# Kernel tuning notes

Measured on AMD Instinct MI355X. Metric: run time of the kernel, lower is better.

The kernel has to match this reference:

```python
import jax, jax.numpy as jnp
import numpy as np

N_NODES = 100000
N_EDGES = 1600000
IN_C, HID_C, OUT_C = 64, 128, 64


def _sage_conv(x, src, dst, Wl, bl, Wr, n_nodes):
    # PyG SAGEConv (mean aggr): out = lin_l(mean_{j in N(i)} x_j) + lin_r(x_i)
    msg = x[src]  # [E, C] gather
    agg = jax.ops.segment_sum(msg, dst, num_segments=n_nodes)
    deg = jax.ops.segment_sum(jnp.ones((src.shape[0],), x.dtype), dst, num_segments=n_nodes)
    agg = agg / jnp.maximum(deg, 1.0)[:, None]
    return agg @ Wl + bl + x @ Wr


def setup_inputs() -> dict:
    key = jax.random.key(0)
    ks = jax.random.split(key, 16)
    x = jax.random.normal(ks[0], (N_NODES, IN_C), dtype=jnp.float32)
    edge_index = jax.random.randint(ks[1], (2, N_EDGES), 0, N_NODES, dtype=jnp.int64)
    s = 0.05
    return {
        "x": x,
        "edge_index": edge_index,
        # conv1: SAGEConv(IN_C, HID_C)
        "Wl1": jax.random.normal(ks[2], (IN_C, HID_C), jnp.float32) * s,
        "bl1": jnp.zeros((HID_C,), jnp.float32),
        "Wr1": jax.random.normal(ks[3], (IN_C, HID_C), jnp.float32) * s,
        # conv2: SAGEConv(HID_C, OUT_C)
        "Wl2": jax.random.normal(ks[4], (HID_C, OUT_C), jnp.float32) * s,
        "bl2": jnp.zeros((OUT_C,), jnp.float32),
        "Wr2": jax.random.normal(ks[5], (HID_C, OUT_C), jnp.float32) * s,
        # classifier MLP: OUT_C -> HID_C -> HID_C//2 -> 1
        "Wc1": jax.random.normal(ks[6], (OUT_C, HID_C), jnp.float32) * s,
        "bc1": jnp.zeros((HID_C,), jnp.float32),
        "Wc2": jax.random.normal(ks[7], (HID_C, HID_C // 2), jnp.float32) * s,
        "bc2": jnp.zeros((HID_C // 2,), jnp.float32),
        "Wc3": jax.random.normal(ks[8], (HID_C // 2, 1), jnp.float32) * s,
        "bc3": jnp.zeros((1,), jnp.float32),
    }


def reference(x, edge_index, Wl1, bl1, Wr1, Wl2, bl2, Wr2, Wc1, bc1, Wc2, bc2, Wc3, bc3):
    src, dst = edge_index[0], edge_index[1]
    n = x.shape[0]
    h = _sage_conv(x, src, dst, Wl1, bl1, Wr1, n)
    h = jax.nn.relu(h)  # dropout is identity in eval mode
    embeddings = _sage_conv(h, src, dst, Wl2, bl2, Wr2, n)
    # classifier head
    c = jax.nn.relu(embeddings @ Wc1 + bc1)
    c = jax.nn.relu(c @ Wc2 + bc2)
    fraud_probs = jax.nn.sigmoid(c @ Wc3 + bc3)
    return embeddings, fraud_probs
```

## Files before the change

kernel.cpp:

```cpp
#include <hip/hip_runtime.h>
#include <math.h>

#define N_NODES 100000
#define N_EDGES 1600000
#define NBKT    391
#define BCAP    5120
#define EPB     4096
#define NBLKA   391

using short8  = __attribute__((ext_vector_type(8))) short;
using float4v = __attribute__((ext_vector_type(4))) float;

__device__ inline unsigned short f2bf(float f) {
    unsigned int u = __float_as_uint(f);
    u += 0x7fffu + ((u >> 16) & 1u);
    return (unsigned short)(u >> 16);
}
__device__ inline float bflo(unsigned int v) { return __uint_as_float(v << 16); }
__device__ inline float bfhi(unsigned int v) { return __uint_as_float(v & 0xffff0000u); }

__global__ void prep_weights(const float* __restrict__ Wl1, const float* __restrict__ Wr1,
                             const float* __restrict__ Wl2, const float* __restrict__ Wr2,
                             const float* __restrict__ Wc1, const float* __restrict__ Wc2,
                             unsigned short* __restrict__ w1, unsigned short* __restrict__ w2,
                             unsigned short* __restrict__ wcls1, unsigned short* __restrict__ wcls2) {
    int i = blockIdx.x * 256 + threadIdx.x;
    if (i < 16384) {
        int n = i >> 7, k = i & 127;
        float v = (k < 64) ? Wl1[k * 128 + n] : Wr1[(k - 64) * 128 + n];
        w1[i] = f2bf(v);
    } else if (i < 32768) {
        int j = i - 16384; int n = j >> 7, k = j & 127;
        float v = (n < 64) ? Wl2[k * 64 + n] : Wr2[k * 64 + (n - 64)];
        w2[j] = f2bf(v);
    } else if (i < 40960) {
        int j = i - 32768; int n = j >> 6, k = j & 63;
        wcls1[j] = f2bf(Wc1[k * 128 + n]);
    } else {
        int j = i - 40960; int n = j >> 7, k = j & 127;
        wcls2[j] = f2bf(Wc2[k * 64 + n]);
    }
}

__global__ void f32_to_bf16x4(const float* __restrict__ src, unsigned short* __restrict__ dst) {
    int i = blockIdx.x * 256 + threadIdx.x;
    float4 v = *(const float4*)(src + (long)i * 4);
    uint2 o;
    o.x = (unsigned)f2bf(v.x) | ((unsigned)f2bf(v.y) << 16);
    o.y = (unsigned)f2bf(v.z) | ((unsigned)f2bf(v.w) << 16);
    *(uint2*)(dst + (long)i * 4) = o;
}

__global__ __launch_bounds__(256) void binA(const int* __restrict__ esrc,
                                            const int* __restrict__ edst,
                                            int* __restrict__ bcnt,
                                            unsigned* __restrict__ stage) {
    __shared__ int hist[NBKT];
    __shared__ int rbase[NBKT];
    int t = threadIdx.x;
    for (int i = t; i < NBKT; i += 256) hist[i] = 0;
    __syncthreads();
    int e0 = blockIdx.x * EPB;
    int e1 = e0 + EPB; if (e1 > N_EDGES) e1 = N_EDGES;
    unsigned pk[16];
    int bn[16];
#pragma unroll
    for (int j = 0; j < 16; j++) {
        int e = e0 + j * 256 + t;
        bn[j] = -1;
        if (e < N_EDGES && e < e1) {
            int d = edst[e];
            int s = esrc[e];
            int b = d >> 8;
            pk[j] = (unsigned)s | ((unsigned)(d & 255) << 24);
            bn[j] = b;
            atomicAdd(&hist[b], 1);
        }
    }
    __syncthreads();
    for (int i = t; i < NBKT; i += 256) {
        int c = hist[i];
        rbase[i] = c ? atomicAdd(&bcnt[i], c) : 0;
        hist[i] = 0;
    }
    __syncthreads();
#pragma unroll
    for (int j = 0; j < 16; j++) {
        if (bn[j] >= 0) {
            int b = bn[j];
            int slot = rbase[b] + atomicAdd(&hist[b], 1);
            if (slot < BCAP)
                stage[(long)b * BCAP + slot] = pk[j];
        }
    }
}

__global__ void binScan(const int* __restrict__ bcnt, int* __restrict__ bbase,
                        int* __restrict__ off) {
    __shared__ int s[512];
    int t = threadIdx.x;
    int v = (t < NBKT) ? bcnt[t] : 0;
    s[t] = v;
    __syncthreads();
    for (int st = 1; st < 512; st <<= 1) {
        int a = (t >= st) ? s[t - st] : 0;
        __syncthreads();
        s[t] += a;
        __syncthreads();
    }
    if (t < NBKT) bbase[t] = s[t] - v;
    if (t == 0) off[N_NODES] = N_EDGES;
}

__global__ __launch_bounds__(256) void binB(const int* __restrict__ bcnt,
                                            const int* __restrict__ bbase,
                                            const unsigned* __restrict__ stage,
                                            int* __restrict__ off, int* __restrict__ bucket) {
    __shared__ int hist[256];
    __shared__ int scn[256];
    __shared__ int lbase[256];
    int b = blockIdx.x, t = threadIdx.x;
    int cnt = bcnt[b];
    if (cnt > BCAP) cnt = BCAP;
    int base = bbase[b];
    hist[t] = 0;
    __syncthreads();
    const unsigned* sp = stage + (long)b * BCAP;
    unsigned pk[20];
    int nv = 0;
#pragma unroll
    for (int j = 0; j < 20; j++) {
        int i = j * 256 + t;
        if (i < cnt) {
            pk[j] = sp[i];
            atomicAdd(&hist[pk[j] >> 24], 1);
            nv = j + 1;
        }
    }
    __syncthreads();
    int v = hist[t];
    scn[t] = v;
    __syncthreads();
    for (int st = 1; st < 256; st <<= 1) {
        int a = (t >= st) ? scn[t - st] : 0;
        __syncthreads();
        scn[t] += a;
        __syncthreads();
    }
    lbase[t] = scn[t] - v;
    int node = b * 256 + t;
    if (node < N_NODES) off[node] = base + lbase[t];
    hist[t] = 0;
    __syncthreads();
#pragma unroll
    for (int j = 0; j < 20; j++) {
        if (j < nv) {
            unsigned p = pk[j];
            int ln = p >> 24;
            int slot = atomicAdd(&hist[ln], 1);
            bucket[base + lbase[ln] + slot] = (int)(p & 0xFFFFFFu);
        }
    }
}

__global__ __launch_bounds__(256, 8) void gather_b(
        const unsigned short* __restrict__ y, const int* __restrict__ off,
        const int* __restrict__ bucket, unsigned short* __restrict__ outb) {
    int node = __builtin_amdgcn_readfirstlane(blockIdx.x * 4 + (threadIdx.x >> 6));
    int lane = threadIdx.x & 63;
    int g = lane >> 3, c8 = lane & 7;
    int e0 = off[node], e1 = off[node + 1];
    float a[8] = {0.f, 0.f, 0.f, 0.f, 0.f, 0.f, 0.f, 0.f};
    for (int base = e0; base < e1; base += 32) {
        uint4 v[4];
#pragma unroll
        for (int h = 0; h < 4; h++) {
            int idx = base + h * 8 + g;
            if (idx < e1) {
                int s = bucket[idx];
                v[h] = *(const uint4*)(y + (long)s * 64 + c8 * 8);
            } else {
                v[h] = (uint4){0u, 0u, 0u, 0u};
            }
        }
#pragma unroll
        for (int h = 0; h < 4; h++) {
            a[0] += bflo(v[h].x); a[1] += bfhi(v[h].x);
            a[2] += bflo(v[h].y); a[3] += bfhi(v[h].y);
            a[4] += bflo(v[h].z); a[5] += bfhi(v[h].z);
            a[6] += bflo(v[h].w); a[7] += bfhi(v[h].w);
        }
    }
#pragma unroll
    for (int j = 0; j < 8; j++) {
        a[j] += __shfl_xor(a[j], 8);
        a[j] += __shfl_xor(a[j], 16);
        a[j] += __shfl_xor(a[j], 32);
    }
    if (g == 0) {
        float sc = 1.f / fmaxf((float)(e1 - e0), 1.f);
        uint4 o;
        o.x = (unsigned)f2bf(a[0]*sc) | ((unsigned)f2bf(a[1]*sc) << 16);
        o.y = (unsigned)f2bf(a[2]*sc) | ((unsigned)f2bf(a[3]*sc) << 16);
        o.z = (unsigned)f2bf(a[4]*sc) | ((unsigned)f2bf(a[5]*sc) << 16);
        o.w = (unsigned)f2bf(a[6]*sc) | ((unsigned)f2bf(a[7]*sc) << 16);
        *(uint4*)(outb + (long)node * 64 + c8 * 8) = o;
    }
}

__global__ __launch_bounds__(256, 8) void gather_badd(
        const unsigned short* __restrict__ y, const int* __restrict__ off,
        const int* __restrict__ bucket, const float* __restrict__ add,
        float* __restrict__ out) {
    int node = __builtin_amdgcn_readfirstlane(blockIdx.x * 4 + (threadIdx.x >> 6));
    int lane = threadIdx.x & 63;
    int g = lane >> 3, c8 = lane & 7;
    int e0 = off[node], e1 = off[node + 1];
    float a[8] = {0.f, 0.f, 0.f, 0.f, 0.f, 0.f, 0.f, 0.f};
    for (int base = e0; base < e1; base += 32) {
        uint4 v[4];
#pragma unroll
        for (int h = 0; h < 4; h++) {
            int idx = base + h * 8 + g;
            if (idx < e1) {
                int s = bucket[idx];
                v[h] = *(const uint4*)(y + (long)s * 64 + c8 * 8);
            } else {
                v[h] = (uint4){0u, 0u, 0u, 0u};
            }
        }
#pragma unroll
        for (int h = 0; h < 4; h++) {
            a[0] += bflo(v[h].x); a[1] += bfhi(v[h].x);
            a[2] += bflo(v[h].y); a[3] += bfhi(v[h].y);
            a[4] += bflo(v[h].z); a[5] += bfhi(v[h].z);
            a[6] += bflo(v[h].w); a[7] += bfhi(v[h].w);
        }
    }
#pragma unroll
    for (int j = 0; j < 8; j++) {
        a[j] += __shfl_xor(a[j], 8);
        a[j] += __shfl_xor(a[j], 16);
        a[j] += __shfl_xor(a[j], 32);
    }
    if (g == 0) {
        float sc = 1.f / fmaxf((float)(e1 - e0), 1.f);
        const float4* up = (const float4*)(add + (long)node * 64 + c8 * 8);
        float4 u0 = up[0], u1 = up[1];
        float4 r0 = { a[0]*sc + u0.x, a[1]*sc + u0.y, a[2]*sc + u0.z, a[3]*sc + u0.w };
        float4 r1 = { a[4]*sc + u1.x, a[5]*sc + u1.y, a[6]*sc + u1.z, a[7]*sc + u1.w };
        float4* op = (float4*)(out + (long)node * 64 + c8 * 8);
        op[0] = r0; op[1] = r1;
    }
}

__global__ __launch_bounds__(256, 4) void fused_conv(
        const unsigned short* __restrict__ xb, const unsigned short* __restrict__ aggb,
        const unsigned short* __restrict__ w1, const float* __restrict__ bl1,
        const unsigned short* __restrict__ w2, const float* __restrict__ bl2,
        unsigned short* __restrict__ t2b, float* __restrict__ u) {
    __shared__ __align__(16) unsigned short smemA[64 * 136];
    __shared__ __align__(16) unsigned short smemH[64 * 136];
    unsigned short* sA = smemA;
    unsigned short* sH = smemH;
    float* su = (float*)smemA;
    unsigned short* st2 = smemH;

    int t = threadIdx.x;
    int lane = t & 63;
    int wv = t >> 6;
    int q = lane >> 4, ln = lane & 15;

    long base = (long)blockIdx.x * 4096;
    long maxe = (long)N_NODES * 64 - 8;
#pragma unroll
    for (int it = 0; it < 2; it++) {
        int i = it * 256 + t;
        int m = i >> 3, k8 = (i & 7) * 8;
        long g = base + (long)m * 64 + k8;
        if (g > maxe) g = maxe;
        *(uint4*)(sA + m * 136 + k8)      = *(const uint4*)(aggb + g);
        *(uint4*)(sA + m * 136 + 64 + k8) = *(const uint4*)(xb + g);
    }
    __syncthreads();

    int n0 = wv * 32;
    float4v acc[2][4];
    {
        float b0 = bl1[n0 + ln], b1 = bl1[n0 + 16 + ln];
#pragma unroll
        for (int mi = 0; mi < 4; mi++) {
            acc[0][mi] = (float4v){b0, b0, b0, b0};
            acc[1][mi] = (float4v){b1, b1, b1, b1};
        }
    }
#pragma unroll
    for (int ks = 0; ks < 4; ks++) {
        int k0 = ks * 32 + q * 8;
        short8 bf0 = *(const short8*)(w1 + (long)(n0 + ln) * 128 + k0);
        short8 bf1 = *(const short8*)(w1 + (long)(n0 + 16 + ln) * 128 + k0);
#pragma unroll
        for (int mi = 0; mi < 4; mi++) {
            short8 af = *(const short8*)(sA + (mi * 16 + ln) * 136 + k0);
            acc[0][mi] = __builtin_amdgcn_mfma_f32_16x16x32_bf16(af, bf0, acc[0][mi], 0, 0, 0);
            acc[1][mi] = __builtin_amdgcn_mfma_f32_16x16x32_bf16(af, bf1, acc[1][mi], 0, 0, 0);
        }
    }
#pragma unroll
    for (int j = 0; j < 2; j++)
#pragma unroll
        for (int mi = 0; mi < 4; mi++) {
            int n = n0 + j * 16 + ln;
#pragma unroll
            for (int r = 0; r < 4; r++) {
                int m = mi * 16 + q * 4 + r;
                sH[m * 136 + n] = f2bf(fmaxf(acc[j][mi][r], 0.f));
            }
        }
    __syncthreads();

    float4v acc2[2][4];
    {
        float c0 = (n0 >= 64) ? bl2[n0 - 64 + ln] : 0.f;
        float c1 = (n0 >= 64) ? bl2[n0 - 48 + ln] : 0.f;
#pragma unroll
        for (int mi = 0; mi < 4; mi++) {
            acc2[0][mi] = (float4v){c0, c0, c0, c0};
            acc2[1][mi] = (float4v){c1, c1, c1, c1};
        }
    }
#pragma unroll
    for (int ks = 0; ks < 4; ks++) {
        int k0 = ks * 32 + q * 8;
        short8 bf0 = *(const short8*)(w2 + (long)(n0 + ln) * 128 + k0);
        short8 bf1 = *(const short8*)(w2 + (long)(n0 + 16 + ln) * 128 + k0);
#pragma unroll
        for (int mi = 0; mi < 4; mi++) {
            short8 af = *(const short8*)(sH + (mi * 16 + ln) * 136 + k0);
            acc2[0][mi] = __builtin_amdgcn_mfma_f32_16x16x32_bf16(af, bf0, acc2[0][mi], 0, 0, 0);
            acc2[1][mi] = __builtin_amdgcn_mfma_f32_16x16x32_bf16(af, bf1, acc2[1][mi], 0, 0, 0);
        }
    }
    __syncthreads();

#pragma unroll
    for (int j = 0; j < 2; j++)
#pragma unroll
        for (int mi = 0; mi < 4; mi++) {
            int n = n0 + j * 16 + ln;
#pragma unroll
            for (int r = 0; r < 4; r++) {
                int m = mi * 16 + q * 4 + r;
                if (wv < 2) st2[m * 72 + n] = f2bf(acc2[j][mi][r]);
                else        su[m * 68 + (n - 64)] = acc2[j][mi][r];
            }
        }
    __syncthreads();

    long lim = (long)N_NODES * 64;
    unsigned int* t2u = (unsigned int*)(t2b + base);
#pragma unroll
    for (int it = 0; it < 8; it++) {
        int i = it * 256 + t;
        long g = base + (long)i * 2;
        if (g + 1 < lim) {
            int m = (i * 2) >> 6, n = (i * 2) & 63;
            t2u[i] = (unsigned)st2[m * 72 + n] | ((unsigned)st2[m * 72 + n + 1] << 16);
        }
    }
#pragma unroll
    for (int it = 0; it < 16; it++) {
        int i = it * 256 + t;
        long g = base + i;
        if (g < lim) u[g] = su[(i >> 6) * 68 + (i & 63)];
    }
}

__global__ __launch_bounds__(256, 4) void fused_cls(
        const float* __restrict__ emb,
        const unsigned short* __restrict__ wcls1, const float* __restrict__ bc1,
        const unsigned short* __restrict__ wcls2, const float* __restrict__ bc2,
        const float* __restrict__ wc3, const float* __restrict__ bc3,
        float* __restrict__ probs) {
    __shared__ __align__(16) unsigned short smem[64 * 136];
    __shared__ float psum[4][64];
    unsigned short* sE = smem;
    unsigned short* sC = smem;

    int t = threadIdx.x;
    int wv = t >> 6;
    int lane = t & 63;
    int q = lane >> 4, ln = lane & 15;

    long base = (long)blockIdx.x * 4096;
    long maxe = (long)N_NODES * 64 - 4;
#pragma unroll
    for (int it = 0; it < 4; it++) {
        int i = it * 256 + t;
        int m = i >> 4, k4 = (i & 15) * 4;
        long g = base + (long)m * 64 + k4;
        if (g > maxe) g = maxe;
        float4 v = *(const float4*)(emb + g);
        uint2 o;
        o.x = (unsigned)f2bf(v.x) | ((unsigned)f2bf(v.y) << 16);
        o.y = (unsigned)f2bf(v.z) | ((unsigned)f2bf(v.w) << 16);
        *(uint2*)(sE + m * 72 + k4) = o;
    }
    __syncthreads();

    int n0 = wv * 32;
    float4v acc[2][4];
    {
        float b0 = bc1[n0 + ln], b1 = bc1[n0 + 16 + ln];
#pragma unroll
        for (int mi = 0; mi < 4; mi++) {
            acc[0][mi] = (float4v){b0, b0, b0, b0};
            acc[1][mi] = (float4v){b1, b1, b1, b1};
        }
    }
#pragma unroll
    for (int ks = 0; ks < 2; ks++) {
        int k0 = ks * 32 + q * 8;
        short8 bf0 = *(const short8*)(wcls1 + (long)(n0 + ln) * 64 + k0);
        short8 bf1 = *(const short8*)(wcls1 + (long)(n0 + 16 + ln) * 64 + k0);
#pragma unroll
        for (int mi = 0; mi < 4; mi++) {
            short8 af = *(const short8*)(sE + (mi * 16 + ln) * 72 + k0);
            acc[0][mi] = __builtin_amdgcn_mfma_f32_16x16x32_bf16(af, bf0, acc[0][mi], 0, 0, 0);
            acc[1][mi] = __builtin_amdgcn_mfma_f32_16x16x32_bf16(af, bf1, acc[1][mi], 0, 0, 0);
        }
    }
    __syncthreads();
#pragma unroll
    for (int j = 0; j < 2; j++)
#pragma unroll
        for (int mi = 0; mi < 4; mi++) {
            int n = n0 + j * 16 + ln;
#pragma unroll
            for (int r = 0; r < 4; r++) {
                int m = mi * 16 + q * 4 + r;
                sC[m * 136 + n] = f2bf(fmaxf(acc[j][mi][r], 0.f));
            }
        }
    __syncthreads();

    int n0c = wv * 16;
    float4v acc3[4];
    {
        float b = bc2[n0c + ln];
#pragma unroll
        for (int mi = 0; mi < 4; mi++) acc3[mi] = (float4v){b, b, b, b};
    }
#pragma unroll
    for (int ks = 0; ks < 4; ks++) {
        int k0 = ks * 32 + q * 8;
        short8 bf0 = *(const short8*)(wcls2 + (long)(n0c + ln) * 128 + k0);
#pragma unroll
        for (int mi = 0; mi < 4; mi++) {
            short8 af = *(const short8*)(sC + (mi * 16 + ln) * 136 + k0);
            acc3[mi] = __builtin_amdgcn_mfma_f32_16x16x32_bf16(af, bf0, acc3[mi], 0, 0, 0);
        }
    }
    float w3 = wc3[n0c + ln];
#pragma unroll
    for (int mi = 0; mi < 4; mi++)
#pragma unroll
        for (int r = 0; r < 4; r++) {
            float v = fmaxf(acc3[mi][r], 0.f) * w3;
            v += __shfl_xor(v, 1);
            v += __shfl_xor(v, 2);
            v += __shfl_xor(v, 4);
            v += __shfl_xor(v, 8);
            if (ln == 0) psum[wv][mi * 16 + q * 4 + r] = v;
        }
    __syncthreads();
    if (t < 64) {
        int node = blockIdx.x * 64 + t;
        if (node < N_NODES) {
            float tot = psum[0][t] + psum[1][t] + psum[2][t] + psum[3][t] + bc3[0];
            probs[node] = 1.f / (1.f + expf(-tot));
        }
    }
}

extern "C" void kernel_launch(void* const* d_in, const int* in_sizes, int n_in,
                              void* d_out, int out_size, void* d_ws, size_t ws_size,
                              hipStream_t stream) {
    const float* x   = (const float*)d_in[0];
    const int*   ei  = (const int*)d_in[1];
    const float* Wl1 = (const float*)d_in[2];
    const float* bl1 = (const float*)d_in[3];
    const float* Wr1 = (const float*)d_in[4];
    const float* Wl2 = (const float*)d_in[5];
    const float* bl2 = (const float*)d_in[6];
    const float* Wr2 = (const float*)d_in[7];
    const float* Wc1 = (const float*)d_in[8];
    const float* bc1 = (const float*)d_in[9];
    const float* Wc2 = (const float*)d_in[10];
    const float* bc2 = (const float*)d_in[11];
    const float* Wc3 = (const float*)d_in[12];
    const float* bc3 = (const float*)d_in[13];

    float* out = (float*)d_out;

    int* iw     = (int*)d_ws;
    int* bcnt   = iw;
    int* bbase  = iw + 392;
    int* off    = iw + 1024;
    int* bucket = iw + 1024 + 100352;
    unsigned* stage = (unsigned*)(iw + 1024 + 100352 + N_EDGES);
    size_t ioff = (size_t)(1024 + 100352 + N_EDGES + (long)NBKT * BCAP) * 4;

    char* wsb = (char*)d_ws;
    unsigned short* xb    = (unsigned short*)(wsb + ioff);
    unsigned short* agg1b = xb + 6400000L;
    unsigned short* t2b   = agg1b + 6400000L;
    float*          u     = (float*)(wsb + ioff + 3L * 12800000L);
    unsigned short* w1    = (unsigned short*)(wsb + ioff + 3L * 12800000L + 25600000L);
    unsigned short* w2    = w1 + 16384;
    unsigned short* wcls1 = w2 + 16384;
    unsigned short* wcls2 = wcls1 + 8192;

    float* emb   = out;
    float* probs = out + 6400000L;

    const int* esrc = ei;
    const int* edst = ei + N_EDGES;

    hipMemsetAsync(bcnt, 0, 1024 * sizeof(int), stream);

    prep_weights<<<192, 256, 0, stream>>>(Wl1, Wr1, Wl2, Wr2, Wc1, Wc2,
                                          w1, w2, wcls1, wcls2);
    f32_to_bf16x4<<<6250, 256, 0, stream>>>(x, xb);

    binA<<<NBLKA, 256, 0, stream>>>(esrc, edst, bcnt, stage);
    binScan<<<1, 512, 0, stream>>>(bcnt, bbase, off);
    binB<<<NBKT, 256, 0, stream>>>(bcnt, bbase, stage, off, bucket);

    gather_b<<<25000, 256, 0, stream>>>(xb, off, bucket, agg1b);
    fused_conv<<<1563, 256, 0, stream>>>(xb, agg1b, w1, bl1, w2, bl2, t2b, u);
    gather_badd<<<25000, 256, 0, stream>>>(t2b, off, bucket, u, emb);
    fused_cls<<<1563, 256, 0, stream>>>(emb, wcls1, bc1, wcls2, bc2, Wc3, bc3, probs);
}
```

Before: 269.6 us.

## Pad per-node edge lists to multiples of eight with a zero sentinel row

The CSR build now pads each node's neighbour list to a multiple of eight, filling the gaps with a sentinel index that points at a zeroed row appended to the bf16 feature buffers, and stores the degree separately. The gather kernels can then test bounds per 8-edge group instead of per lane and use 32-bit byte offsets for the row loads. The weight-prep and x-conversion kernels are merged into one launch, which also zeroes the sentinel rows. This adds padding loads of zero rows and a larger bucket buffer in exchange for simpler, branch-uniform gather loops.

```diff
diff --git a/kernel.cpp b/kernel.cpp
--- a/kernel.cpp
+++ b/kernel.cpp
@@ -2,11 +2,14 @@
 #include <math.h>
 
 #define N_NODES 100000
+#define ZERO_NODE 100000
 #define N_EDGES 1600000
 #define NBKT    391
 #define BCAP    5120
 #define EPB     4096
 #define NBLKA   391
+#define PADBKT  1792
+#define BUCKET_CAP (N_EDGES + NBKT * PADBKT)
 
 using short8  = __attribute__((ext_vector_type(8))) short;
 using float4v = __attribute__((ext_vector_type(4))) float;
@@ -19,36 +22,43 @@
 __device__ inline float bflo(unsigned int v) { return __uint_as_float(v << 16); }
 __device__ inline float bfhi(unsigned int v) { return __uint_as_float(v & 0xffff0000u); }
 
-__global__ void prep_weights(const float* __restrict__ Wl1, const float* __restrict__ Wr1,
-                             const float* __restrict__ Wl2, const float* __restrict__ Wr2,
-                             const float* __restrict__ Wc1, const float* __restrict__ Wc2,
-                             unsigned short* __restrict__ w1, unsigned short* __restrict__ w2,
-                             unsigned short* __restrict__ wcls1, unsigned short* __restrict__ wcls2) {
-    int i = blockIdx.x * 256 + threadIdx.x;
-    if (i < 16384) {
-        int n = i >> 7, k = i & 127;
-        float v = (k < 64) ? Wl1[k * 128 + n] : Wr1[(k - 64) * 128 + n];
-        w1[i] = f2bf(v);
-    } else if (i < 32768) {
-        int j = i - 16384; int n = j >> 7, k = j & 127;
-        float v = (n < 64) ? Wl2[k * 64 + n] : Wr2[k * 64 + (n - 64)];
-        w2[j] = f2bf(v);
-    } else if (i < 40960) {
-        int j = i - 32768; int n = j >> 6, k = j & 63;
-        wcls1[j] = f2bf(Wc1[k * 128 + n]);
+__global__ void prep_all(const float* __restrict__ x, unsigned short* __restrict__ xb,
+                         const float* __restrict__ Wl1, const float* __restrict__ Wr1,
+                         const float* __restrict__ Wl2, const float* __restrict__ Wr2,
+                         const float* __restrict__ Wc1, const float* __restrict__ Wc2,
+                         unsigned short* __restrict__ w1, unsigned short* __restrict__ w2,
+                         unsigned short* __restrict__ wcls1, unsigned short* __restrict__ wcls2,
+                         unsigned short* __restrict__ t2b) {
+    int bid = blockIdx.x;
+    int t = threadIdx.x;
+    if (bid < 6250) {
+        int i = bid * 256 + t;
+        float4 v = *(const float4*)(x + (long)i * 4);
+        uint2 o;
+        o.x = (unsigned)f2bf(v.x) | ((unsigned)f2bf(v.y) << 16);
+        o.y = (unsigned)f2bf(v.z) | ((unsigned)f2bf(v.w) << 16);
+        *(uint2*)(xb + (long)i * 4) = o;
+    } else if (bid < 6442) {
+        int i = (bid - 6250) * 256 + t;
+        if (i < 16384) {
+            int n = i >> 7, k = i & 127;
+            float v = (k < 64) ? Wl1[k * 128 + n] : Wr1[(k - 64) * 128 + n];
+            w1[i] = f2bf(v);
+        } else if (i < 32768) {
+            int j = i - 16384; int n = j >> 7, k = j & 127;
+            float v = (n < 64) ? Wl2[k * 64 + n] : Wr2[k * 64 + (n - 64)];
+            w2[j] = f2bf(v);
+        } else if (i < 40960) {
+            int j = i - 32768; int n = j >> 6, k = j & 63;
+            wcls1[j] = f2bf(Wc1[k * 128 + n]);
+        } else {
+            int j = i - 40960; int n = j >> 7, k = j & 127;
+            wcls2[j] = f2bf(Wc2[k * 64 + n]);
+        }
     } else {
-        int j = i - 40960; int n = j >> 7, k = j & 127;
-        wcls2[j] = f2bf(Wc2[k * 64 + n]);
-    }
-}
-
-__global__ void f32_to_bf16x4(const float* __restrict__ src, unsigned short* __restrict__ dst) {
-    int i = blockIdx.x * 256 + threadIdx.x;
-    float4 v = *(const float4*)(src + (long)i * 4);
-    uint2 o;
-    o.x = (unsigned)f2bf(v.x) | ((unsigned)f2bf(v.y) << 16);
-    o.y = (unsigned)f2bf(v.z) | ((unsigned)f2bf(v.w) << 16);
-    *(uint2*)(dst + (long)i * 4) = o;
+        if (t < 32)       ((unsigned*)(xb  + (long)ZERO_NODE * 64))[t]      = 0u;
+        else if (t < 64)  ((unsigned*)(t2b + (long)ZERO_NODE * 64))[t - 32] = 0u;
+    }
 }
 
 __global__ __launch_bounds__(256) void binA(const int* __restrict__ esrc,
@@ -95,8 +105,7 @@
     }
 }
 
-__global__ void binScan(const int* __restrict__ bcnt, int* __restrict__ bbase,
-                        int* __restrict__ off) {
+__global__ void binScan(const int* __restrict__ bcnt, int* __restrict__ pbase) {
     __shared__ int s[512];
     int t = threadIdx.x;
     int v = (t < NBKT) ? bcnt[t] : 0;
@@ -108,21 +117,21 @@
         s[t] += a;
         __syncthreads();
     }
-    if (t < NBKT) bbase[t] = s[t] - v;
-    if (t == 0) off[N_NODES] = N_EDGES;
+    if (t < NBKT) pbase[t] = (s[t] - v) + t * PADBKT;
 }
 
 __global__ __launch_bounds__(256) void binB(const int* __restrict__ bcnt,
-                                            const int* __restrict__ bbase,
+                                            const int* __restrict__ pbase,
                                             const unsigned* __restrict__ stage,
-                                            int* __restrict__ off, int* __restrict__ bucket) {
+                                            int* __restrict__ offp, int* __restrict__ deg,
+                                            int* __restrict__ bucket) {
     __shared__ int hist[256];
     __shared__ int scn[256];
     __shared__ int lbase[256];
     int b = blockIdx.x, t = threadIdx.x;
     int cnt = bcnt[b];
     if (cnt > BCAP) cnt = BCAP;
-    int base = bbase[b];
+    int base = pbase[b];
     hist[t] = 0;
     __syncthreads();
     const unsigned* sp = stage + (long)b * BCAP;
@@ -139,7 +148,8 @@
     }
     __syncthreads();
     int v = hist[t];
-    scn[t] = v;
+    int p8 = (v + 7) & ~7;
+    scn[t] = p8;
     __syncthreads();
     for (int st = 1; st < 256; st <<= 1) {
         int a = (t >= st) ? scn[t - st] : 0;
@@ -147,9 +157,12 @@
         scn[t] += a;
         __syncthreads();
     }
-    lbase[t] = scn[t] - v;
+    lbase[t] = scn[t] - p8;
     int node = b * 256 + t;
-    if (node < N_NODES) off[node] = base + lbase[t];
+    if (node < N_NODES) {
+        offp[node] = base + lbase[t];
+        deg[node]  = v;
+    }
     hist[t] = 0;
     __syncthreads();
 #pragma unroll
@@ -161,24 +174,31 @@
             bucket[base + lbase[ln] + slot] = (int)(p & 0xFFFFFFu);
         }
     }
+    int ps = base + lbase[t] + v;
+    int pe = base + lbase[t] + p8;
+    for (int j = ps; j < pe; j++) bucket[j] = ZERO_NODE;
 }
 
 __global__ __launch_bounds__(256, 8) void gather_b(
-        const unsigned short* __restrict__ y, const int* __restrict__ off,
-        const int* __restrict__ bucket, unsigned short* __restrict__ outb) {
+        const unsigned short* __restrict__ y, const int* __restrict__ offp,
+        const int* __restrict__ deg, const int* __restrict__ bucket,
+        unsigned short* __restrict__ outb) {
     int node = __builtin_amdgcn_readfirstlane(blockIdx.x * 4 + (threadIdx.x >> 6));
     int lane = threadIdx.x & 63;
     int g = lane >> 3, c8 = lane & 7;
-    int e0 = off[node], e1 = off[node + 1];
+    int e0 = offp[node];
+    int dg = deg[node];
+    int e1p = e0 + ((dg + 7) & ~7);
+    const char* yb = (const char*)y;
     float a[8] = {0.f, 0.f, 0.f, 0.f, 0.f, 0.f, 0.f, 0.f};
-    for (int base = e0; base < e1; base += 32) {
+    for (int base = e0; base < e1p; base += 32) {
         uint4 v[4];
 #pragma unroll
         for (int h = 0; h < 4; h++) {
-            int idx = base + h * 8 + g;
-            if (idx < e1) {
-                int s = bucket[idx];
-                v[h] = *(const uint4*)(y + (long)s * 64 + c8 * 8);
+            if (base + h * 8 < e1p) {
+                int s = bucket[base + h * 8 + g];
+                unsigned off32 = ((unsigned)s << 7) + ((unsigned)c8 << 4);
+                v[h] = *(const uint4*)(yb + off32);
             } else {
                 v[h] = (uint4){0u, 0u, 0u, 0u};
             }
@@ -198,7 +218,7 @@
         a[j] += __shfl_xor(a[j], 32);
     }
     if (g == 0) {
-        float sc = 1.f / fmaxf((float)(e1 - e0), 1.f);
+        float sc = 1.f / fmaxf((float)dg, 1.f);
         uint4 o;
         o.x = (unsigned)f2bf(a[0]*sc) | ((unsigned)f2bf(a[1]*sc) << 16);
         o.y = (unsigned)f2bf(a[2]*sc) | ((unsigned)f2bf(a[3]*sc) << 16);
@@ -209,22 +229,25 @@
 }
 
 __global__ __launch_bounds__(256, 8) void gather_badd(
-        const unsigned short* __restrict__ y, const int* __restrict__ off,
-        const int* __restrict__ bucket, const float* __restrict__ add,
-        float* __restrict__ out) {
+        const unsigned short* __restrict__ y, const int* __restrict__ offp,
+        const int* __restrict__ deg, const int* __restrict__ bucket,
+        const float* __restrict__ add, float* __restrict__ out) {
     int node = __builtin_amdgcn_readfirstlane(blockIdx.x * 4 + (threadIdx.x >> 6));
     int lane = threadIdx.x & 63;
     int g = lane >> 3, c8 = lane & 7;
-    int e0 = off[node], e1 = off[node + 1];
+    int e0 = offp[node];
+    int dg = deg[node];
+    int e1p = e0 + ((dg + 7) & ~7);
+    const char* yb = (const char*)y;
     float a[8] = {0.f, 0.f, 0.f, 0.f, 0.f, 0.f, 0.f, 0.f};
-    for (int base = e0; base < e1; base += 32) {
+    for (int base = e0; base < e1p; base += 32) {
         uint4 v[4];
 #pragma unroll
         for (int h = 0; h < 4; h++) {
-            int idx = base + h * 8 + g;
-            if (idx < e1) {
-                int s = bucket[idx];
-                v[h] = *(const uint4*)(y + (long)s * 64 + c8 * 8);
+            if (base + h * 8 < e1p) {
+                int s = bucket[base + h * 8 + g];
+                unsigned off32 = ((unsigned)s << 7) + ((unsigned)c8 << 4);
+                v[h] = *(const uint4*)(yb + off32);
             } else {
                 v[h] = (uint4){0u, 0u, 0u, 0u};
             }
@@ -244,7 +267,7 @@
         a[j] += __shfl_xor(a[j], 32);
     }
     if (g == 0) {
-        float sc = 1.f / fmaxf((float)(e1 - e0), 1.f);
+        float sc = 1.f / fmaxf((float)dg, 1.f);
         const float4* up = (const float4*)(add + (long)node * 64 + c8 * 8);
         float4 u0 = up[0], u1 = up[1];
         float4 r0 = { a[0]*sc + u0.x, a[1]*sc + u0.y, a[2]*sc + u0.z, a[3]*sc + u0.w };
@@ -505,18 +528,20 @@
 
     int* iw     = (int*)d_ws;
     int* bcnt   = iw;
-    int* bbase  = iw + 392;
-    int* off    = iw + 1024;
-    int* bucket = iw + 1024 + 100352;
-    unsigned* stage = (unsigned*)(iw + 1024 + 100352 + N_EDGES);
-    size_t ioff = (size_t)(1024 + 100352 + N_EDGES + (long)NBKT * BCAP) * 4;
+    int* pbase  = iw + 512;
+    int* offp   = iw + 1024;
+    int* deg    = iw + 1024 + 100352;
+    int* bucket = iw + 1024 + 2 * 100352;
+    unsigned* stage = (unsigned*)(bucket + BUCKET_CAP);
+    size_t ioff = ((size_t)(1024 + 2 * 100352 + BUCKET_CAP) + (size_t)NBKT * BCAP) * 4;
+    ioff = (ioff + 127) & ~(size_t)127;
 
     char* wsb = (char*)d_ws;
     unsigned short* xb    = (unsigned short*)(wsb + ioff);
-    unsigned short* agg1b = xb + 6400000L;
+    unsigned short* agg1b = xb + 6400064L;
     unsigned short* t2b   = agg1b + 6400000L;
-    float*          u     = (float*)(wsb + ioff + 3L * 12800000L);
-    unsigned short* w1    = (unsigned short*)(wsb + ioff + 3L * 12800000L + 25600000L);
+    float*          u     = (float*)(t2b + 6400064L);
+    unsigned short* w1    = (unsigned short*)(u + 6400000L);
     unsigned short* w2    = w1 + 16384;
     unsigned short* wcls1 = w2 + 16384;
     unsigned short* wcls2 = wcls1 + 8192;
@@ -529,16 +554,15 @@
 
     hipMemsetAsync(bcnt, 0, 1024 * sizeof(int), stream);
 
-    prep_weights<<<192, 256, 0, stream>>>(Wl1, Wr1, Wl2, Wr2, Wc1, Wc2,
-                                          w1, w2, wcls1, wcls2);
-    f32_to_bf16x4<<<6250, 256, 0, stream>>>(x, xb);
+    prep_all<<<6443, 256, 0, stream>>>(x, xb, Wl1, Wr1, Wl2, Wr2, Wc1, Wc2,
+                                       w1, w2, wcls1, wcls2, t2b);
 
     binA<<<NBLKA, 256, 0, stream>>>(esrc, edst, bcnt, stage);
-    binScan<<<1, 512, 0, stream>>>(bcnt, bbase, off);
-    binB<<<NBKT, 256, 0, stream>>>(bcnt, bbase, stage, off, bucket);
-
-    gather_b<<<25000, 256, 0, stream>>>(xb, off, bucket, agg1b);
+    binScan<<<1, 512, 0, stream>>>(bcnt, pbase);
+    binB<<<NBKT, 256, 0, stream>>>(bcnt, pbase, stage, offp, deg, bucket);
+
+    gather_b<<<25000, 256, 0, stream>>>(xb, offp, deg, bucket, agg1b);
     fused_conv<<<1563, 256, 0, stream>>>(xb, agg1b, w1, bl1, w2, bl2, t2b, u);
-    gather_badd<<<25000, 256, 0, stream>>>(t2b, off, bucket, u, emb);
+    gather_badd<<<25000, 256, 0, stream>>>(t2b, offp, deg, bucket, u, emb);
     fused_cls<<<1563, 256, 0, stream>>>(emb, wcls1, bc1, wcls2, bc2, Wc3, bc3, probs);
 }
```

After: 269.8 us. About the same (+0.1%).
